# Optimization experiments

Hardware: AMD Instinct MI355X
Metric: run time of the kernel (lower is better)

## Reference

```python
import jax, jax.numpy as jnp
import numpy as np

B, T, N, D, H, O, A = 16, 64, 128, 512, 512, 256, 18  # batch, time, graph_size, obs_dim, gcn_hidden, gcn_out, num_outputs


def setup_inputs() -> dict:
    key = jax.random.key(0)
    ks = jax.random.split(key, 10)
    s = 0.02
    return {
        "obs": jax.random.normal(ks[0], (B * T, D), jnp.float32),
        "nodes": jnp.zeros((B, N, D), jnp.float32),
        "num_nodes": jnp.zeros((B,), jnp.int32),
        "adj": jnp.zeros((B, N, N), jnp.int32),
        "W1": jax.random.normal(ks[1], (D, H), jnp.float32) * s,
        "b1": jnp.zeros((H,), jnp.float32),
        "W2": jax.random.normal(ks[2], (H, O), jnp.float32) * s,
        "b2": jnp.zeros((O,), jnp.float32),
        "Wl": jax.random.normal(ks[3], (O, A), jnp.float32) * s,
        "bl": jnp.zeros((A,), jnp.float32),
        "Wv": jax.random.normal(ks[4], (O, 1), jnp.float32) * s,
        "bv": jnp.zeros((1,), jnp.float32),
    }


def gcn(x, adjf, W, b):
    # GCNConv with add_self_loops=True: A_hat = A | I, sym-normalized.
    n = adjf.shape[-1]
    Ahat = jnp.maximum(adjf, jnp.eye(n, dtype=adjf.dtype))  # [B,N,N]
    dinv = jax.lax.rsqrt(Ahat.sum(-1))                      # deg >= 1 always
    An = dinv[..., :, None] * Ahat * dinv[..., None, :]
    return jnp.einsum('bij,bjh->bih', An, x @ W) + b


def reference(obs, nodes, num_nodes, adj, W1, b1, W2, b2, Wl, bl, Wv, bv):
    Bv = num_nodes.shape[0]
    Tv = obs.shape[0] // Bv
    flat = obs.reshape(Bv, Tv, -1).transpose(1, 0, 2)  # [T,B,D]
    bidx = jnp.arange(Bv)

    def step(carry, x_t):
        nn_, nd, ad = carry
        nn_ = jnp.where(nn_ == N - 1, 0, nn_)              # graph overflow reset
        nd = nd.at[bidx, nn_].set(x_t)                     # write obs into node buffer
        ad = ad.at[bidx, nn_, nn_].set(1)                  # self edge
        back = (nn_ > 1).astype(ad.dtype)                  # temporal backedge only if num_nodes > 1
        ad = ad.at[bidx, nn_, nn_ - 1].max(back)
        ad = ad.at[bidx, nn_ - 1, nn_].max(back)
        adjf = ad.astype(x_t.dtype)
        h = jax.nn.relu(gcn(nd, adjf, W1, b1))
        h = jax.nn.relu(gcn(h, adjf, W2, b2))
        tgt = h[bidx, nn_]                                 # [B,O] current node embedding
        logit = tgt @ Wl + bl
        val = tgt @ Wv + bv
        return (nn_ + 1, nd, ad), (logit, val)

    _, (logits, values) = jax.lax.scan(step, (num_nodes, nodes, adj), flat)
    logits = logits.transpose(1, 0, 2).reshape(Bv * Tv, -1)  # [B*T, A]
    return logits
```

## Files before the change

### kernel.cpp

```cpp
#include <hip/hip_runtime.h>

#define DD 512
#define HH 512
#define OO 256
#define AA 18
#define ROWS 1024

typedef __attribute__((ext_vector_type(8))) short bf16x8;
typedef __attribute__((ext_vector_type(4))) float f32x4;

__device__ __forceinline__ unsigned short f2bf(float x) {
  unsigned u = __builtin_bit_cast(unsigned, x);
  u += 0x7FFFu + ((u >> 16) & 1u);
  return (unsigned short)(u >> 16);
}

__global__ __launch_bounds__(512) void k1_mfma_combine(
    const float* __restrict__ obs, const float* __restrict__ W1,
    const float* __restrict__ b1, const float* __restrict__ W2,
    unsigned short* __restrict__ U, unsigned short* __restrict__ W2t,
    float* __restrict__ out) {
  __shared__ unsigned short As[2][64][72];
  __shared__ unsigned short Bt[2][32][72];
  __shared__ float Gs[2][64][36];

  const int tid = threadIdx.x;
  const int blk = blockIdx.x;
  const int g = tid >> 8;
  const int gt = tid & 255;
  const int lane = tid & 63;
  const int wid = (tid >> 6) & 3;
  const int col0 = (blk & 15) * 32;
  const int row0 = (blk >> 4) * 64;
  const int k0 = g * 256;

  if (tid < 72) out[blk * 72 + tid] = 0.f;
  W2t[(size_t)blk * HH + tid] = f2bf(W2[(size_t)tid * OO + blk]);

  const int sar = gt >> 2, sak = (gt & 3) * 16;
  const int sbc = gt & 31, sbk = (gt >> 5) * 8;
  const int lr = lane & 15, lk = (lane >> 4) * 8;

  float4 pa0, pa1, pa2, pa3;
  float pb0, pb1, pb2, pb3, pb4, pb5, pb6, pb7;
  f32x4 acc0 = {0.f, 0.f, 0.f, 0.f}, acc1 = {0.f, 0.f, 0.f, 0.f};

#define LOADG(kb)                                                              \
  {                                                                            \
    const float* Ap = &obs[(size_t)(row0 + sar) * DD + (kb) + sak];            \
    pa0 = *reinterpret_cast<const float4*>(Ap);                                \
    pa1 = *reinterpret_cast<const float4*>(Ap + 4);                            \
    pa2 = *reinterpret_cast<const float4*>(Ap + 8);                            \
    pa3 = *reinterpret_cast<const float4*>(Ap + 12);                           \
    const float* Bp = &W1[(size_t)((kb) + sbk) * HH + col0 + sbc];             \
    pb0 = Bp[0]; pb1 = Bp[HH]; pb2 = Bp[2 * HH]; pb3 = Bp[3 * HH];             \
    pb4 = Bp[4 * HH]; pb5 = Bp[5 * HH]; pb6 = Bp[6 * HH]; pb7 = Bp[7 * HH];    \
  }
#define STOLDS()                                                               \
  {                                                                            \
    bf16x8 v0, v1;                                                             \
    v0[0] = (short)f2bf(pa0.x); v0[1] = (short)f2bf(pa0.y);                    \
    v0[2] = (short)f2bf(pa0.z); v0[3] = (short)f2bf(pa0.w);                    \
    v0[4] = (short)f2bf(pa1.x); v0[5] = (short)f2bf(pa1.y);                    \
    v0[6] = (short)f2bf(pa1.z); v0[7] = (short)f2bf(pa1.w);                    \
    v1[0] = (short)f2bf(pa2.x); v1[1] = (short)f2bf(pa2.y);                    \
    v1[2] = (short)f2bf(pa2.z); v1[3] = (short)f2bf(pa2.w);                    \
    v1[4] = (short)f2bf(pa3.x); v1[5] = (short)f2bf(pa3.y);                    \
    v1[6] = (short)f2bf(pa3.z); v1[7] = (short)f2bf(pa3.w);                    \
    *reinterpret_cast<bf16x8*>(&As[g][sar][sak]) = v0;                         \
    *reinterpret_cast<bf16x8*>(&As[g][sar][sak + 8]) = v1;                     \
    bf16x8 w;                                                                  \
    w[0] = (short)f2bf(pb0); w[1] = (short)f2bf(pb1);                          \
    w[2] = (short)f2bf(pb2); w[3] = (short)f2bf(pb3);                          \
    w[4] = (short)f2bf(pb4); w[5] = (short)f2bf(pb5);                          \
    w[6] = (short)f2bf(pb6); w[7] = (short)f2bf(pb7);                          \
    *reinterpret_cast<bf16x8*>(&Bt[g][sbc][sbk]) = w;                          \
  }
#define COMPUTE()                                                              \
  {                                                                            \
    _Pragma("unroll") for (int ks = 0; ks < 2; ++ks) {                         \
      const bf16x8 af =                                                        \
          *reinterpret_cast<const bf16x8*>(&As[g][wid * 16 + lr][ks * 32 + lk]); \
      const bf16x8 bf0 =                                                       \
          *reinterpret_cast<const bf16x8*>(&Bt[g][lr][ks * 32 + lk]);          \
      const bf16x8 bf1 =                                                       \
          *reinterpret_cast<const bf16x8*>(&Bt[g][16 + lr][ks * 32 + lk]);     \
      acc0 = __builtin_amdgcn_mfma_f32_16x16x32_bf16(af, bf0, acc0, 0, 0, 0);  \
      acc1 = __builtin_amdgcn_mfma_f32_16x16x32_bf16(af, bf1, acc1, 0, 0, 0);  \
    }                                                                          \
  }

  LOADG(k0);
  STOLDS();
  __syncthreads();
  for (int tt = 1; tt < 4; ++tt) {
    LOADG(k0 + tt * 64);
    COMPUTE();
    __syncthreads();
    STOLDS();
    __syncthreads();
  }
  COMPUTE();
  __syncthreads();
#undef LOADG
#undef STOLDS
#undef COMPUTE

  {
    const int crow = wid * 16 + (lane >> 4) * 4;
#pragma unroll
    for (int i = 0; i < 4; ++i) Gs[g][crow + i][lr] = acc0[i];
#pragma unroll
    for (int i = 0; i < 4; ++i) Gs[g][crow + i][16 + lr] = acc1[i];
  }
  __syncthreads();

  {
    const int rr = tid >> 3;
    const int c4 = (tid & 7) * 4;
    const int t = rr;
    const float is6 = 0.4082482904638630f;
    float c0, c1, c2, d1, d2, al, be;
    if (t <= 1) {
      c0 = 0.f; c1 = 0.f; c2 = 1.f; d1 = 0.f; d2 = 0.f; al = 1.f; be = 0.f;
    } else if (t == 2) {
      c0 = 0.f; c1 = 0.5f; c2 = 0.5f; d1 = 0.5f; d2 = 0.5f; al = 0.5f; be = 0.5f;
    } else {
      c0 = (t == 3) ? is6 : (1.f / 3.f);
      c1 = 1.f / 3.f; c2 = is6;
      d1 = is6; d2 = 0.5f;
      al = is6; be = 0.5f;
    }
    const int rm1 = (t >= 1) ? rr - 1 : rr;
    const int rm2 = (t >= 2) ? rr - 2 : rr;
    ushort4 uo;
    unsigned short* up = (unsigned short*)&uo;
#pragma unroll
    for (int j = 0; j < 4; ++j) {
      const int c = c4 + j;
      const float gc = Gs[0][rr][c] + Gs[1][rr][c];
      const float gb = Gs[0][rm1][c] + Gs[1][rm1][c];
      const float ga = Gs[0][rm2][c] + Gs[1][rm2][c];
      const float bb = b1[col0 + c];
      const float h1a = fmaxf(c0 * ga + c1 * gb + c2 * gc + bb, 0.f);
      const float h1b = fmaxf(d1 * gb + d2 * gc + bb, 0.f);
      up[j] = f2bf(al * h1a + be * h1b);
    }
    *reinterpret_cast<ushort4*>(&U[(size_t)(row0 + rr) * HH + col0 + c4]) = uo;
  }
}

__global__ __launch_bounds__(256) void k2_fused_head(
    const unsigned short* __restrict__ U, const unsigned short* __restrict__ W2t,
    const float* __restrict__ b2, const float* __restrict__ Wl,
    const float* __restrict__ bl, float* __restrict__ out) {
  __shared__ unsigned short As2[32][136];
  __shared__ unsigned short Bt2[32][136];
  __shared__ float tg[32][36];
  __shared__ float sWl[32][18];

  const int tid = threadIdx.x;
  const int lane = tid & 63;
  const int w = tid >> 6;
  const int rt2 = w & 1, nt2 = w >> 1;
  const int ct = blockIdx.x & 7;
  const int col0 = ct * 32;
  const int r0 = (blockIdx.x >> 3) * 32;
  const int lr = lane & 15, lk = (lane >> 4) * 8;

  const int sar = tid >> 3, sak = (tid & 7) * 16;
  const int sbn = tid & 31, sbk = (tid >> 5) * 16;

  bf16x8 pa0, pa1, pb0, pb1;
  f32x4 acc = {0.f, 0.f, 0.f, 0.f};

#define LOADG(kb)                                                              \
  {                                                                            \
    const unsigned short* Ap = &U[(size_t)(r0 + sar) * HH + (kb) + sak];       \
    pa0 = *reinterpret_cast<const bf16x8*>(Ap);                                \
    pa1 = *reinterpret_cast<const bf16x8*>(Ap + 8);                            \
    const unsigned short* Bp = &W2t[(size_t)(col0 + sbn) * HH + (kb) + sbk];   \
    pb0 = *reinterpret_cast<const bf16x8*>(Bp);                                \
    pb1 = *reinterpret_cast<const bf16x8*>(Bp + 8);                            \
  }
#define STOLDS()                                                               \
  {                                                                            \
    *reinterpret_cast<bf16x8*>(&As2[sar][sak]) = pa0;                          \
    *reinterpret_cast<bf16x8*>(&As2[sar][sak + 8]) = pa1;                      \
    *reinterpret_cast<bf16x8*>(&Bt2[sbn][sbk]) = pb0;                          \
    *reinterpret_cast<bf16x8*>(&Bt2[sbn][sbk + 8]) = pb1;                      \
  }
#define COMPUTE()                                                              \
  {                                                                            \
    _Pragma("unroll") for (int ks = 0; ks < 4; ++ks) {                         \
      const bf16x8 af =                                                        \
          *reinterpret_cast<const bf16x8*>(&As2[rt2 * 16 + lr][ks * 32 + lk]); \
      const bf16x8 bf =                                                        \
          *reinterpret_cast<const bf16x8*>(&Bt2[nt2 * 16 + lr][ks * 32 + lk]); \
      acc = __builtin_amdgcn_mfma_f32_16x16x32_bf16(af, bf, acc, 0, 0, 0);     \
    }                                                                          \
  }

  LOADG(0);
  STOLDS();
  __syncthreads();
  for (int tt = 1; tt < 4; ++tt) {
    LOADG(tt * 128);
    COMPUTE();
    __syncthreads();
    STOLDS();
    __syncthreads();
  }
  COMPUTE();
  __syncthreads();
#undef LOADG
#undef STOLDS
#undef COMPUTE

  {
    const int crow = rt2 * 16 + (lane >> 4) * 4;
#pragma unroll
    for (int i = 0; i < 4; ++i) tg[crow + i][nt2 * 16 + lr] = acc[i];
  }
  for (int i = tid; i < 32 * AA; i += 256) {
    const int n = i / AA, o = i - n * AA;
    sWl[n][o] = Wl[(size_t)(col0 + n) * AA + o];
  }
  __syncthreads();

  for (int i = tid; i < 32 * 32; i += 256) {
    const int r = i >> 5, c = i & 31;
    tg[r][c] = fmaxf(tg[r][c] + b2[col0 + c], 0.f);
  }
  __syncthreads();

  for (int p = tid; p < 32 * AA; p += 256) {
    const int r = p / AA, o = p - r * AA;
    float s = (ct == 0) ? bl[o] : 0.f;
#pragma unroll 8
    for (int n = 0; n < 32; ++n) s = fmaf(tg[r][n], sWl[n][o], s);
    atomicAdd(&out[(size_t)(r0 + r) * AA + o], s);
  }
}

extern "C" void kernel_launch(void* const* d_in, const int* in_sizes, int n_in,
                              void* d_out, int out_size, void* d_ws, size_t ws_size,
                              hipStream_t stream) {
  const float* obs = (const float*)d_in[0];
  const float* W1 = (const float*)d_in[4];
  const float* b1 = (const float*)d_in[5];
  const float* W2 = (const float*)d_in[6];
  const float* b2 = (const float*)d_in[7];
  const float* Wl = (const float*)d_in[8];
  const float* bl = (const float*)d_in[9];
  float* out = (float*)d_out;

  unsigned short* U = (unsigned short*)d_ws;
  unsigned short* W2t = U + (size_t)ROWS * HH;

  k1_mfma_combine<<<256, 512, 0, stream>>>(obs, W1, b1, W2, U, W2t, out);

  k2_fused_head<<<256, 256, 0, stream>>>(U, W2t, b2, Wl, bl, out);
}
```

Before: 18.61 us.

## Split K across wave pairs in head GEMM kernel with shared-memory reduction

The second kernel now runs 512 threads per block. Its K dimension of 512 is split into four 128-wide slices, one per wave pair, and all slices are loaded into shared memory in a single stage. The earlier serial four-step load/compute loop and its barriers are gone, and the partial sums are reduced through shared memory before bias, ReLU and the logit head. This trades more shared memory and more threads per block for a shorter serial dependency chain and fewer synchronisations per block.

Result: faster. 16.94 us (-9.0%).

```diff
diff --git a/kernel.cpp b/kernel.cpp
--- a/kernel.cpp
+++ b/kernel.cpp
@@ -150,95 +150,85 @@
   }
 }
 
-__global__ __launch_bounds__(256) void k2_fused_head(
+__global__ __launch_bounds__(512) void k2_fused_head(
     const unsigned short* __restrict__ U, const unsigned short* __restrict__ W2t,
     const float* __restrict__ b2, const float* __restrict__ Wl,
     const float* __restrict__ bl, float* __restrict__ out) {
-  __shared__ unsigned short As2[32][136];
-  __shared__ unsigned short Bt2[32][136];
-  __shared__ float tg[32][36];
+  __shared__ unsigned short As2[4][32][136];
+  __shared__ unsigned short Bt2[4][32][136];
+  __shared__ float tg[4][32][36];
+  __shared__ float tgs[32][36];
   __shared__ float sWl[32][18];
 
   const int tid = threadIdx.x;
   const int lane = tid & 63;
   const int w = tid >> 6;
-  const int rt2 = w & 1, nt2 = w >> 1;
+  const int kg = w >> 1;
+  const int wg = w & 1;
+  const int gt = tid & 127;
   const int ct = blockIdx.x & 7;
   const int col0 = ct * 32;
   const int r0 = (blockIdx.x >> 3) * 32;
   const int lr = lane & 15, lk = (lane >> 4) * 8;
-
-  const int sar = tid >> 3, sak = (tid & 7) * 16;
-  const int sbn = tid & 31, sbk = (tid >> 5) * 16;
-
-  bf16x8 pa0, pa1, pb0, pb1;
-  f32x4 acc = {0.f, 0.f, 0.f, 0.f};
-
-#define LOADG(kb)                                                              \
-  {                                                                            \
-    const unsigned short* Ap = &U[(size_t)(r0 + sar) * HH + (kb) + sak];       \
-    pa0 = *reinterpret_cast<const bf16x8*>(Ap);                                \
-    pa1 = *reinterpret_cast<const bf16x8*>(Ap + 8);                            \
-    const unsigned short* Bp = &W2t[(size_t)(col0 + sbn) * HH + (kb) + sbk];   \
-    pb0 = *reinterpret_cast<const bf16x8*>(Bp);                                \
-    pb1 = *reinterpret_cast<const bf16x8*>(Bp + 8);                            \
-  }
-#define STOLDS()                                                               \
-  {                                                                            \
-    *reinterpret_cast<bf16x8*>(&As2[sar][sak]) = pa0;                          \
-    *reinterpret_cast<bf16x8*>(&As2[sar][sak + 8]) = pa1;                      \
-    *reinterpret_cast<bf16x8*>(&Bt2[sbn][sbk]) = pb0;                          \
-    *reinterpret_cast<bf16x8*>(&Bt2[sbn][sbk + 8]) = pb1;                      \
-  }
-#define COMPUTE()                                                              \
-  {                                                                            \
-    _Pragma("unroll") for (int ks = 0; ks < 4; ++ks) {                         \
-      const bf16x8 af =                                                        \
-          *reinterpret_cast<const bf16x8*>(&As2[rt2 * 16 + lr][ks * 32 + lk]); \
-      const bf16x8 bf =                                                        \
-          *reinterpret_cast<const bf16x8*>(&Bt2[nt2 * 16 + lr][ks * 32 + lk]); \
-      acc = __builtin_amdgcn_mfma_f32_16x16x32_bf16(af, bf, acc, 0, 0, 0);     \
-    }                                                                          \
-  }
-
-  LOADG(0);
-  STOLDS();
-  __syncthreads();
-  for (int tt = 1; tt < 4; ++tt) {
-    LOADG(tt * 128);
-    COMPUTE();
-    __syncthreads();
-    STOLDS();
-    __syncthreads();
-  }
-  COMPUTE();
-  __syncthreads();
-#undef LOADG
-#undef STOLDS
-#undef COMPUTE
-
-  {
-    const int crow = rt2 * 16 + (lane >> 4) * 4;
-#pragma unroll
-    for (int i = 0; i < 4; ++i) tg[crow + i][nt2 * 16 + lr] = acc[i];
-  }
-  for (int i = tid; i < 32 * AA; i += 256) {
+  const int k0 = kg * 128;
+
+  const int sar = gt >> 2, sak = (gt & 3) * 32;
+
+  for (int i = tid; i < 32 * AA; i += 512) {
     const int n = i / AA, o = i - n * AA;
     sWl[n][o] = Wl[(size_t)(col0 + n) * AA + o];
   }
-  __syncthreads();
-
-  for (int i = tid; i < 32 * 32; i += 256) {
+
+  bf16x8 pa[4], pb[4];
+  {
+    const unsigned short* Ap = &U[(size_t)(r0 + sar) * HH + k0 + sak];
+#pragma unroll
+    for (int q = 0; q < 4; ++q) pa[q] = *reinterpret_cast<const bf16x8*>(Ap + q * 8);
+    const unsigned short* Bp = &W2t[(size_t)(col0 + sar) * HH + k0 + sak];
+#pragma unroll
+    for (int q = 0; q < 4; ++q) pb[q] = *reinterpret_cast<const bf16x8*>(Bp + q * 8);
+  }
+#pragma unroll
+  for (int q = 0; q < 4; ++q)
+    *reinterpret_cast<bf16x8*>(&As2[kg][sar][sak + q * 8]) = pa[q];
+#pragma unroll
+  for (int q = 0; q < 4; ++q)
+    *reinterpret_cast<bf16x8*>(&Bt2[kg][sar][sak + q * 8]) = pb[q];
+  __syncthreads();
+
+  f32x4 acc0 = {0.f, 0.f, 0.f, 0.f}, acc1 = {0.f, 0.f, 0.f, 0.f};
+#pragma unroll
+  for (int ks = 0; ks < 4; ++ks) {
+    const bf16x8 af = *reinterpret_cast<const bf16x8*>(&As2[kg][wg * 16 + lr][ks * 32 + lk]);
+    const bf16x8 bf0 = *reinterpret_cast<const bf16x8*>(&Bt2[kg][lr][ks * 32 + lk]);
+    const bf16x8 bf1 = *reinterpret_cast<const bf16x8*>(&Bt2[kg][16 + lr][ks * 32 + lk]);
+    acc0 = __builtin_amdgcn_mfma_f32_16x16x32_bf16(af, bf0, acc0, 0, 0, 0);
+    acc1 = __builtin_amdgcn_mfma_f32_16x16x32_bf16(af, bf1, acc1, 0, 0, 0);
+  }
+
+  {
+    const int crow = wg * 16 + (lane >> 4) * 4;
+#pragma unroll
+    for (int i = 0; i < 4; ++i) {
+      tg[kg][crow + i][lr] = acc0[i];
+      tg[kg][crow + i][16 + lr] = acc1[i];
+    }
+  }
+  __syncthreads();
+
+  for (int i = tid; i < 32 * 32; i += 512) {
     const int r = i >> 5, c = i & 31;
-    tg[r][c] = fmaxf(tg[r][c] + b2[col0 + c], 0.f);
-  }
-  __syncthreads();
-
-  for (int p = tid; p < 32 * AA; p += 256) {
+    const float s = tg[0][r][c] + tg[1][r][c] + tg[2][r][c] + tg[3][r][c]
+                    + b2[col0 + c];
+    tgs[r][c] = fmaxf(s, 0.f);
+  }
+  __syncthreads();
+
+  for (int p = tid; p < 32 * AA; p += 512) {
     const int r = p / AA, o = p - r * AA;
     float s = (ct == 0) ? bl[o] : 0.f;
 #pragma unroll 8
-    for (int n = 0; n < 32; ++n) s = fmaf(tg[r][n], sWl[n][o], s);
+    for (int n = 0; n < 32; ++n) s = fmaf(tgs[r][n], sWl[n][o], s);
     atomicAdd(&out[(size_t)(r0 + r) * AA + o], s);
   }
 }
@@ -260,5 +250,5 @@
 
   k1_mfma_combine<<<256, 512, 0, stream>>>(obs, W1, b1, W2, U, W2t, out);
 
-  k2_fused_head<<<256, 256, 0, stream>>>(U, W2t, b2, Wl, bl, out);
-}
+  k2_fused_head<<<256, 512, 0, stream>>>(U, W2t, b2, Wl, bl, out);
+}
```
